# Kernel optimization log

Hardware: AMD Instinct MI355X
Metric: run time of the kernel (lower is better)

The kernel has to match this reference:

```python
import jax, jax.numpy as jnp
import numpy as np

B, S, D = 2, 2048, 2048
H, HKV = 16, 2
DH = D // H          # 128
G = H // HKV         # 8
SCALE = float(np.sqrt(DH))


def setup_inputs() -> dict:
    key = jax.random.key(0)
    ks = jax.random.split(key, 9)
    s = 0.02
    return {
        "x":  jax.random.normal(ks[0], (B, S, D), dtype=jnp.float32),
        "Wq": jax.random.normal(ks[1], (H * DH, D), dtype=jnp.float32) * s,
        "bq": jnp.zeros((H * DH,), dtype=jnp.float32),
        "Wk": jax.random.normal(ks[2], (HKV * DH, D), dtype=jnp.float32) * s,
        "bk": jnp.zeros((HKV * DH,), dtype=jnp.float32),
        "Wv": jax.random.normal(ks[3], (HKV * DH, D), dtype=jnp.float32) * s,
        "bv": jnp.zeros((HKV * DH,), dtype=jnp.float32),
        "Wo": jax.random.normal(ks[4], (D, D), dtype=jnp.float32) * s,
        "bo": jnp.zeros((D,), dtype=jnp.float32),
    }


def reference(x, Wq, bq, Wk, bk, Wv, bv, Wo, bo):
    # projections (torch Linear: y = x @ W.T + b)
    q = (x @ Wq.T + bq).reshape(B, S, HKV, G, DH)   # grouped query heads
    k = (x @ Wk.T + bk).reshape(B, S, HKV, DH)
    v = (x @ Wv.T + bv).reshape(B, S, HKV, DH)

    # scores: [B, HKV, G, S, S]; native grouping (no KV expand/copy)
    scores = jnp.einsum('bskgd,btkd->bkgst', q, k) / SCALE

    causal = jnp.triu(jnp.ones((S, S), dtype=bool), k=1)
    scores = jnp.where(causal, -jnp.inf, scores)
    attn = jax.nn.softmax(scores, axis=-1)          # dropout = identity (eval)

    out = jnp.einsum('bkgst,btkd->bskgd', attn, v).reshape(B, S, D)
    return out @ Wo.T + bo
```

## Files before the change

### kernel.cpp

```cpp
#include <hip/hip_runtime.h>
#include <hip/hip_bf16.h>
#include <cmath>
#include <stdint.h>

#define B_ 2
#define S_ 2048
#define D_ 2048
#define H_ 16
#define HKV_ 2
#define DH_ 128
#define G_ 8
#define DKV_ 256
#define NQKV_ 2560

typedef _Float16 f16;
typedef _Float16 f16x8 __attribute__((ext_vector_type(8)));
typedef _Float16 f16x4 __attribute__((ext_vector_type(4)));
typedef float f32x4 __attribute__((ext_vector_type(4)));

__device__ __forceinline__ void gload_lds16(const void* g, void* lds) {
  __builtin_amdgcn_global_load_lds((const __attribute__((address_space(1))) void*)g,
                                   (__attribute__((address_space(3))) void*)lds,
                                   16, 0, 0);
}

__device__ __forceinline__ float fexp2(float x) {
  float r;
  asm("v_exp_f32 %0, %1" : "=v"(r) : "v"(x));
  return r;
}

__global__ void prep_kernel(const float* __restrict__ x,  const float* __restrict__ Wq,
                            const float* __restrict__ Wk, const float* __restrict__ Wv,
                            const float* __restrict__ Wo, const float* __restrict__ bq,
                            const float* __restrict__ bk, const float* __restrict__ bv,
                            f16* __restrict__ xh, f16* __restrict__ wqkv,
                            f16* __restrict__ woh, float* __restrict__ bqkv) {
  constexpr int N0 = 2097152;
  constexpr int N1 = N0 + 1048576;
  constexpr int N2 = N1 + 131072;
  constexpr int N3 = N2 + 131072;
  constexpr int N4 = N3 + 1048576;
  constexpr int N5 = N4 + 512;
  constexpr int N6 = N5 + 64;
  constexpr int N7 = N6 + 64;
  int i = blockIdx.x * blockDim.x + threadIdx.x;
  const int stride = gridDim.x * blockDim.x;
  for (; i < N7; i += stride) {
    if (i < N4) {
      const float* s; f16x4* d; int j;
      if (i < N0)      { s = x;  d = (f16x4*)xh;             j = i; }
      else if (i < N1) { s = Wq; d = (f16x4*)wqkv;           j = i - N0; }
      else if (i < N2) { s = Wk; d = (f16x4*)wqkv + 1048576; j = i - N1; }
      else if (i < N3) { s = Wv; d = (f16x4*)wqkv + 1179648; j = i - N2; }
      else             { s = Wo; d = (f16x4*)woh;            j = i - N3; }
      float4 v = reinterpret_cast<const float4*>(s)[j];
      f16x4 o = { (f16)v.x, (f16)v.y, (f16)v.z, (f16)v.w };
      d[j] = o;
    } else {
      const float* s; int off, j;
      if (i < N5)      { s = bq; off = 0;   j = i - N4; }
      else if (i < N6) { s = bk; off = 512; j = i - N5; }
      else             { s = bv; off = 576; j = i - N6; }
      reinterpret_cast<float4*>(bqkv)[off + j] = reinterpret_cast<const float4*>(s)[j];
    }
  }
}

template<int EPI>
__global__ __launch_bounds__(256)
void gemm_core(const f16* __restrict__ A, const f16* __restrict__ Bm,
               const float* __restrict__ bias,
               f16* __restrict__ oQ, f16* __restrict__ oK, f16* __restrict__ oV,
               float* __restrict__ oF,
               int M, int N, int K, int nbx) {
  __shared__ __align__(16) f16 sA[128 * 64];
  __shared__ __align__(16) f16 sB[128 * 64];
  const int tid  = threadIdx.x;
  const int lane = tid & 63;
  const int w    = tid >> 6;
  const int wr   = w >> 1, wc = w & 1;
  const int r16  = lane & 15, grp = lane >> 4;
  const int nwg  = gridDim.x;
  const int cpx  = nwg >> 3;
  const int lg   = (blockIdx.x & 7) * cpx + (blockIdx.x >> 3);
  const int bm   = (lg / nbx) * 128;
  const int bn   = (lg % nbx) * 128;

  f32x4 acc[4][4] = {};

  auto stage = [&](int k0) {
#pragma unroll
    for (int j = 0; j < 4; ++j) {
      int seg = j * 4 + w;
      int rr  = seg * 8 + (lane >> 3);
      int cs  = lane & 7;
      int csr = (cs ^ (rr & 7)) * 8;
      gload_lds16(A  + (size_t)(bm + rr) * K + k0 + csr, &sA[seg * 512]);
      gload_lds16(Bm + (size_t)(bn + rr) * K + k0 + csr, &sB[seg * 512]);
    }
  };

  const int nk = K >> 6;
  for (int t = 0; t < nk; ++t) {
    stage(t << 6);
    asm volatile("s_waitcnt vmcnt(0)" ::: "memory");
    __builtin_amdgcn_s_barrier();

#pragma unroll
    for (int kk = 0; kk < 64; kk += 32) {
      f16x8 af[4], bf[4];
      const int cb = (kk >> 3) + grp;
      const int cx = (cb ^ (r16 & 7)) << 3;
#pragma unroll
      for (int m = 0; m < 4; ++m)
        af[m] = *reinterpret_cast<const f16x8*>(&sA[(wr * 64 + m * 16 + r16) * 64 + cx]);
#pragma unroll
      for (int n = 0; n < 4; ++n)
        bf[n] = *reinterpret_cast<const f16x8*>(&sB[(wc * 64 + n * 16 + r16) * 64 + cx]);
#pragma unroll
      for (int m = 0; m < 4; ++m)
#pragma unroll
        for (int n = 0; n < 4; ++n)
          acc[m][n] = __builtin_amdgcn_mfma_f32_16x16x32_f16(af[m], bf[n], acc[m][n], 0, 0, 0);
    }

    __builtin_amdgcn_s_barrier();
  }

#pragma unroll
  for (int n = 0; n < 4; ++n) {
    int col = bn + wc * 64 + n * 16 + r16;
    float bv = bias ? bias[col] : 0.f;
#pragma unroll
    for (int m = 0; m < 4; ++m) {
      int row0 = bm + wr * 64 + m * 16 + grp * 4;
      if constexpr (EPI == 0) {
#pragma unroll
        for (int j = 0; j < 4; ++j)
          oF[(size_t)(row0 + j) * N + col] = acc[m][n][j] + bv;
      } else {
        if (bn < 2048) {
#pragma unroll
          for (int j = 0; j < 4; ++j)
            oQ[(size_t)(row0 + j) * 2048 + col] = (f16)(acc[m][n][j] + bv);
        } else if (bn < 2304) {
#pragma unroll
          for (int j = 0; j < 4; ++j)
            oK[(size_t)(row0 + j) * 256 + (col - 2048)] = (f16)(acc[m][n][j] + bv);
        } else {
          f16x4 st;
#pragma unroll
          for (int j = 0; j < 4; ++j) st[j] = (f16)(acc[m][n][j] + bv);
          *reinterpret_cast<f16x4*>(&oV[(size_t)(row0 >> 2) * 1024 + (col - 2304) * 4]) = st;
        }
      }
    }
  }
}

__global__ __launch_bounds__(256)
void attn_kernel(const f16* __restrict__ Q, const f16* __restrict__ K,
                 const f16* __restrict__ V4, f16* __restrict__ O) {
  __shared__ __align__(16) f16 sK[2][8192];
  __shared__ __align__(16) f16 sV[2][8192];

  const int tid  = threadIdx.x;
  const int lane = tid & 63;
  const int w    = tid >> 6;
  const int qi   = lane & 15, grp = lane >> 4;
  const int bid  = blockIdx.x;
  const int hh   = bid & 1;
  const int kvh  = (bid >> 1) & 1;
  const int b    = (bid >> 2) & 1;
  const int j    = bid >> 3;
  const int hq   = kvh * 8 + hh * 4 + w;
  const f16 SCL2 = (f16)(0.08838834764831845f * 1.44269504088896f);

  const f16* Kb = K  + (size_t)b * S_ * DKV_ + kvh * DH_;
  const f16* Vb = V4 + (size_t)b * S_ * DKV_ + kvh * 512;

  auto stage = [&](int t64, int buf) {
#pragma unroll
    for (int p4 = 0; p4 < 4; ++p4) {
      int ci = p4 * 256 + tid;
      int r = ci >> 4, cs = ci & 15;
      gload_lds16(Kb + (size_t)(t64 * 64 + r) * DKV_ + ((cs ^ (r & 7)) * 8),
                  (char*)&sK[buf][0] + p4 * 4096 + w * 1024);
      int g = ci >> 6, cc = ci & 63;
      gload_lds16(Vb + (size_t)(t64 * 16 + g) * 1024 + ((cc ^ g) * 8),
                  (char*)&sV[buf][0] + p4 * 4096 + w * 1024);
    }
  };

  const int q2    = qi >> 1;
  const int voff0 = ((q2 ^ grp) << 3) + (qi & 1) * 4;
  const int voff1 = ((q2 ^ (grp + 4)) << 3) + (qi & 1) * 4;

  for (int task = 0; task < 2; ++task) {
    const int qt    = task ? j : (127 - j);
    const int nt    = (qt >> 2) + 1;
    const int q_pos = qt * 16 + qi;

    const size_t qbase = ((size_t)(b * S_ + qt * 16 + qi)) * D_ + hq * DH_;
    f16x8 qf[4];
#pragma unroll
    for (int kd = 0; kd < 4; ++kd) {
      qf[kd] = *reinterpret_cast<const f16x8*>(Q + qbase + kd * 32 + grp * 8);
#pragma unroll
      for (int e = 0; e < 8; ++e) qf[kd][e] *= SCL2;
    }

    float m = -INFINITY, lsum = 0.f;
    f32x4 accO[8] = {};

    auto tile_step = [&](const f16* sKb, const f16* sVb, int kv0, bool MASK) {
      f32x4 s0 = {}, s1 = {}, s2 = {}, s3 = {};
#pragma unroll
      for (int kd = 0; kd < 4; ++kd) {
        const int cx = ((kd * 4 + grp) ^ (qi & 7)) << 3;
        f16x8 k0 = *reinterpret_cast<const f16x8*>(sKb + qi * 128 + cx);
        f16x8 k1 = *reinterpret_cast<const f16x8*>(sKb + (16 + qi) * 128 + cx);
        f16x8 k2 = *reinterpret_cast<const f16x8*>(sKb + (32 + qi) * 128 + cx);
        f16x8 k3 = *reinterpret_cast<const f16x8*>(sKb + (48 + qi) * 128 + cx);
        s0 = __builtin_amdgcn_mfma_f32_16x16x32_f16(k0, qf[kd], s0, 0, 0, 0);
        s1 = __builtin_amdgcn_mfma_f32_16x16x32_f16(k1, qf[kd], s1, 0, 0, 0);
        s2 = __builtin_amdgcn_mfma_f32_16x16x32_f16(k2, qf[kd], s2, 0, 0, 0);
        s3 = __builtin_amdgcn_mfma_f32_16x16x32_f16(k3, qf[kd], s3, 0, 0, 0);
      }
      float p[16];
#pragma unroll
      for (int jj = 0; jj < 4; ++jj) {
        p[jj] = s0[jj]; p[4 + jj] = s1[jj]; p[8 + jj] = s2[jj]; p[12 + jj] = s3[jj];
      }
      if (MASK) {
#pragma unroll
        for (int qd = 0; qd < 4; ++qd)
#pragma unroll
          for (int jj = 0; jj < 4; ++jj) {
            int kvp = kv0 + qd * 16 + grp * 4 + jj;
            p[qd * 4 + jj] = (kvp > q_pos) ? -INFINITY : p[qd * 4 + jj];
          }
      }
      float a0 = fmaxf(p[0], p[8]),  a1 = fmaxf(p[1], p[9]);
      float a2 = fmaxf(p[2], p[10]), a3 = fmaxf(p[3], p[11]);
      float a4 = fmaxf(p[4], p[12]), a5 = fmaxf(p[5], p[13]);
      float a6 = fmaxf(p[6], p[14]), a7 = fmaxf(p[7], p[15]);
      a0 = fmaxf(a0, a4); a1 = fmaxf(a1, a5); a2 = fmaxf(a2, a6); a3 = fmaxf(a3, a7);
      a0 = fmaxf(a0, a2); a1 = fmaxf(a1, a3);
      float tm = fmaxf(a0, a1);
      if (!__all(tm <= m + 8.f)) {
        float r = tm;
        r = fmaxf(r, __shfl_xor(r, 16));
        r = fmaxf(r, __shfl_xor(r, 32));
        float mn = fmaxf(m, r);
        float sc = fexp2(m - mn);
        m = mn;
        lsum *= sc;
#pragma unroll
        for (int dt = 0; dt < 8; ++dt)
#pragma unroll
          for (int jj = 0; jj < 4; ++jj) accO[dt][jj] *= sc;
      }
      float ps = 0.f;
#pragma unroll
      for (int i = 0; i < 16; ++i) {
        p[i] = fexp2(p[i] - m);
        ps += p[i];
      }
      lsum += ps;

      f16x4 pf0 = { (f16)p[0],  (f16)p[1],  (f16)p[2],  (f16)p[3]  };
      f16x4 pf1 = { (f16)p[4],  (f16)p[5],  (f16)p[6],  (f16)p[7]  };
      f16x4 pf2 = { (f16)p[8],  (f16)p[9],  (f16)p[10], (f16)p[11] };
      f16x4 pf3 = { (f16)p[12], (f16)p[13], (f16)p[14], (f16)p[15] };
      const f16* vb0 = sVb + grp * 512 + voff0;
      const f16* vb1 = sVb + (grp + 4) * 512 + voff1;
      const f16* vb2 = sVb + (8 + grp) * 512 + voff0;
      const f16* vb3 = sVb + (12 + grp) * 512 + voff1;
#pragma unroll
      for (int dtp = 0; dtp < 8; ++dtp) {
        const int dt1 = dtp ^ 1;
        f16x4 v0 = *reinterpret_cast<const f16x4*>(vb0 + dtp * 64);
        f16x4 v1 = *reinterpret_cast<const f16x4*>(vb1 + dtp * 64);
        f16x4 v2 = *reinterpret_cast<const f16x4*>(vb2 + dtp * 64);
        f16x4 v3 = *reinterpret_cast<const f16x4*>(vb3 + dtp * 64);
        accO[dtp] = __builtin_amdgcn_mfma_f32_16x16x16f16(v0, pf0, accO[dtp], 0, 0, 0);
        accO[dtp] = __builtin_amdgcn_mfma_f32_16x16x16f16(v1, pf1, accO[dtp], 0, 0, 0);
        accO[dt1] = __builtin_amdgcn_mfma_f32_16x16x16f16(v2, pf2, accO[dt1], 0, 0, 0);
        accO[dt1] = __builtin_amdgcn_mfma_f32_16x16x16f16(v3, pf3, accO[dt1], 0, 0, 0);
      }
    };

    stage(0, 0);
    asm volatile("s_waitcnt vmcnt(0)" ::: "memory");
    __builtin_amdgcn_s_barrier();

    for (int t = 0; t < nt - 1; ++t) {
      const int buf = t & 1;
      stage(t + 1, buf ^ 1);
      tile_step(&sK[buf][0], &sV[buf][0], t * 64, false);
      asm volatile("s_waitcnt vmcnt(0)" ::: "memory");
      __builtin_amdgcn_s_barrier();
    }

    {
      const int t = nt - 1, buf = t & 1;
      tile_step(&sK[buf][0], &sV[buf][0], t * 64, true);
    }

    lsum += __shfl_xor(lsum, 16);
    lsum += __shfl_xor(lsum, 32);
    float inv_l = 1.f / lsum;
    const size_t obase = ((size_t)(b * S_ + qt * 16 + qi)) * D_ + hq * DH_;
#pragma unroll
    for (int dt = 0; dt < 8; ++dt) {
      f16x4 st;
#pragma unroll
      for (int jj = 0; jj < 4; ++jj) st[jj] = (f16)(accO[dt][jj] * inv_l);
      *reinterpret_cast<f16x4*>(&O[obase + dt * 16 + grp * 4]) = st;
    }
    __builtin_amdgcn_s_barrier();
  }
}

extern "C" void kernel_launch(void* const* d_in, const int* in_sizes, int n_in,
                              void* d_out, int out_size, void* d_ws, size_t ws_size,
                              hipStream_t stream) {
  const float* x  = (const float*)d_in[0];
  const float* Wq = (const float*)d_in[1];
  const float* bq = (const float*)d_in[2];
  const float* Wk = (const float*)d_in[3];
  const float* bk = (const float*)d_in[4];
  const float* Wv = (const float*)d_in[5];
  const float* bv = (const float*)d_in[6];
  const float* Wo = (const float*)d_in[7];
  const float* bo = (const float*)d_in[8];
  float* out = (float*)d_out;

  char* ws = (char*)d_ws;
  size_t off = 0;
  auto alloc = [&](size_t bytes) {
    char* p = ws + off;
    off += (bytes + 255) & ~(size_t)255;
    return p;
  };
  f16*   xh    = (f16*)alloc((size_t)B_ * S_ * D_ * 2);
  f16*   wqkv  = (f16*)alloc((size_t)NQKV_ * D_ * 2);
  f16*   woh   = (f16*)alloc((size_t)D_ * D_ * 2);
  f16*   qh    = (f16*)alloc((size_t)B_ * S_ * D_ * 2);
  f16*   kh    = (f16*)alloc((size_t)B_ * S_ * DKV_ * 2);
  f16*   v4h   = (f16*)alloc((size_t)B_ * S_ * DKV_ * 2);
  f16*   ah    = (f16*)alloc((size_t)B_ * S_ * D_ * 2);
  float* bqkv  = (float*)alloc((size_t)NQKV_ * 4);

  prep_kernel<<<dim3(2048), dim3(256), 0, stream>>>(
      x, Wq, Wk, Wv, Wo, bq, bk, bv, xh, wqkv, woh, bqkv);

  const int M = B_ * S_;
  gemm_core<1><<<dim3((M / 128) * (NQKV_ / 128)), 256, 0, stream>>>(
      xh, wqkv, bqkv, qh, kh, v4h, nullptr, M, NQKV_, D_, NQKV_ / 128);

  attn_kernel<<<dim3(512), 256, 0, stream>>>(qh, kh, v4h, ah);

  gemm_core<0><<<dim3((M / 128) * (D_ / 128)), 256, 0, stream>>>(
      ah, woh, bo, nullptr, nullptr, nullptr, out, M, D_, D_, D_ / 128);
}
```

Measured before the change: 184.5 us.

## Process two query heads per wave to reuse K/V tiles across heads

Each wave now handles two query heads of the same KV group. The K and V fragments read from shared memory feed both heads' MFMAs, so each block stages a KV tile once for all 8 grouped heads instead of twice. The per-block pair of complementary causal tasks is dropped. Instead the block index is remapped so one block handles one query tile, with long and short tiles interleaved across the grid. This halves LDS reads and global K/V traffic per head, at the cost of doubling accumulator registers (which may lower occupancy) and giving up the explicit per-block causal load balancing.

```diff
diff --git a/kernel.cpp b/kernel.cpp
--- a/kernel.cpp
+++ b/kernel.cpp
@@ -170,11 +170,12 @@
   const int w    = tid >> 6;
   const int qi   = lane & 15, grp = lane >> 4;
   const int bid  = blockIdx.x;
-  const int hh   = bid & 1;
-  const int kvh  = (bid >> 1) & 1;
-  const int b    = (bid >> 2) & 1;
-  const int j    = bid >> 3;
-  const int hq   = kvh * 8 + hh * 4 + w;
+  const int b    = (bid >> 1) & 1;
+  const int kvh  = (bid >> 2) & 1;
+  const int v_   = ((bid >> 3) & 31) * 2 + (bid & 1);
+  const int qt   = (bid & 256) ? (127 - v_) : v_;
+  const int hqA  = kvh * 8 + w;
+  const int hqB  = kvh * 8 + 4 + w;
   const f16 SCL2 = (f16)(0.08838834764831845f * 1.44269504088896f);
 
   const f16* Kb = K  + (size_t)b * S_ * DKV_ + kvh * DH_;
@@ -197,130 +198,157 @@
   const int voff0 = ((q2 ^ grp) << 3) + (qi & 1) * 4;
   const int voff1 = ((q2 ^ (grp + 4)) << 3) + (qi & 1) * 4;
 
-  for (int task = 0; task < 2; ++task) {
-    const int qt    = task ? j : (127 - j);
-    const int nt    = (qt >> 2) + 1;
-    const int q_pos = qt * 16 + qi;
-
-    const size_t qbase = ((size_t)(b * S_ + qt * 16 + qi)) * D_ + hq * DH_;
-    f16x8 qf[4];
+  const int nt    = (qt >> 2) + 1;
+  const int q_pos = qt * 16 + qi;
+
+  const size_t qrow = ((size_t)(b * S_ + qt * 16 + qi)) * D_;
+  f16x8 qfA[4], qfB[4];
+#pragma unroll
+  for (int kd = 0; kd < 4; ++kd) {
+    qfA[kd] = *reinterpret_cast<const f16x8*>(Q + qrow + hqA * DH_ + kd * 32 + grp * 8);
+    qfB[kd] = *reinterpret_cast<const f16x8*>(Q + qrow + hqB * DH_ + kd * 32 + grp * 8);
+#pragma unroll
+    for (int e = 0; e < 8; ++e) { qfA[kd][e] *= SCL2; qfB[kd][e] *= SCL2; }
+  }
+
+  float mA = -INFINITY, lsA = 0.f;
+  float mB = -INFINITY, lsB = 0.f;
+  f32x4 accA[8] = {}, accB[8] = {};
+
+  auto tile_step = [&](const f16* sKb, const f16* sVb, int kv0, bool MASK) {
+    f32x4 sA0 = {}, sA1 = {}, sA2 = {}, sA3 = {};
+    f32x4 sB0 = {}, sB1 = {}, sB2 = {}, sB3 = {};
 #pragma unroll
     for (int kd = 0; kd < 4; ++kd) {
-      qf[kd] = *reinterpret_cast<const f16x8*>(Q + qbase + kd * 32 + grp * 8);
-#pragma unroll
-      for (int e = 0; e < 8; ++e) qf[kd][e] *= SCL2;
-    }
-
-    float m = -INFINITY, lsum = 0.f;
-    f32x4 accO[8] = {};
-
-    auto tile_step = [&](const f16* sKb, const f16* sVb, int kv0, bool MASK) {
-      f32x4 s0 = {}, s1 = {}, s2 = {}, s3 = {};
-#pragma unroll
-      for (int kd = 0; kd < 4; ++kd) {
-        const int cx = ((kd * 4 + grp) ^ (qi & 7)) << 3;
-        f16x8 k0 = *reinterpret_cast<const f16x8*>(sKb + qi * 128 + cx);
-        f16x8 k1 = *reinterpret_cast<const f16x8*>(sKb + (16 + qi) * 128 + cx);
-        f16x8 k2 = *reinterpret_cast<const f16x8*>(sKb + (32 + qi) * 128 + cx);
-        f16x8 k3 = *reinterpret_cast<const f16x8*>(sKb + (48 + qi) * 128 + cx);
-        s0 = __builtin_amdgcn_mfma_f32_16x16x32_f16(k0, qf[kd], s0, 0, 0, 0);
-        s1 = __builtin_amdgcn_mfma_f32_16x16x32_f16(k1, qf[kd], s1, 0, 0, 0);
-        s2 = __builtin_amdgcn_mfma_f32_16x16x32_f16(k2, qf[kd], s2, 0, 0, 0);
-        s3 = __builtin_amdgcn_mfma_f32_16x16x32_f16(k3, qf[kd], s3, 0, 0, 0);
-      }
-      float p[16];
-#pragma unroll
-      for (int jj = 0; jj < 4; ++jj) {
-        p[jj] = s0[jj]; p[4 + jj] = s1[jj]; p[8 + jj] = s2[jj]; p[12 + jj] = s3[jj];
-      }
-      if (MASK) {
-#pragma unroll
-        for (int qd = 0; qd < 4; ++qd)
-#pragma unroll
-          for (int jj = 0; jj < 4; ++jj) {
-            int kvp = kv0 + qd * 16 + grp * 4 + jj;
-            p[qd * 4 + jj] = (kvp > q_pos) ? -INFINITY : p[qd * 4 + jj];
-          }
-      }
-      float a0 = fmaxf(p[0], p[8]),  a1 = fmaxf(p[1], p[9]);
-      float a2 = fmaxf(p[2], p[10]), a3 = fmaxf(p[3], p[11]);
-      float a4 = fmaxf(p[4], p[12]), a5 = fmaxf(p[5], p[13]);
-      float a6 = fmaxf(p[6], p[14]), a7 = fmaxf(p[7], p[15]);
+      const int cx = ((kd * 4 + grp) ^ (qi & 7)) << 3;
+      f16x8 k0 = *reinterpret_cast<const f16x8*>(sKb + qi * 128 + cx);
+      f16x8 k1 = *reinterpret_cast<const f16x8*>(sKb + (16 + qi) * 128 + cx);
+      f16x8 k2 = *reinterpret_cast<const f16x8*>(sKb + (32 + qi) * 128 + cx);
+      f16x8 k3 = *reinterpret_cast<const f16x8*>(sKb + (48 + qi) * 128 + cx);
+      sA0 = __builtin_amdgcn_mfma_f32_16x16x32_f16(k0, qfA[kd], sA0, 0, 0, 0);
+      sB0 = __builtin_amdgcn_mfma_f32_16x16x32_f16(k0, qfB[kd], sB0, 0, 0, 0);
+      sA1 = __builtin_amdgcn_mfma_f32_16x16x32_f16(k1, qfA[kd], sA1, 0, 0, 0);
+      sB1 = __builtin_amdgcn_mfma_f32_16x16x32_f16(k1, qfB[kd], sB1, 0, 0, 0);
+      sA2 = __builtin_amdgcn_mfma_f32_16x16x32_f16(k2, qfA[kd], sA2, 0, 0, 0);
+      sB2 = __builtin_amdgcn_mfma_f32_16x16x32_f16(k2, qfB[kd], sB2, 0, 0, 0);
+      sA3 = __builtin_amdgcn_mfma_f32_16x16x32_f16(k3, qfA[kd], sA3, 0, 0, 0);
+      sB3 = __builtin_amdgcn_mfma_f32_16x16x32_f16(k3, qfB[kd], sB3, 0, 0, 0);
+    }
+    float pA[16], pB[16];
+#pragma unroll
+    for (int jj = 0; jj < 4; ++jj) {
+      pA[jj] = sA0[jj]; pA[4 + jj] = sA1[jj]; pA[8 + jj] = sA2[jj]; pA[12 + jj] = sA3[jj];
+      pB[jj] = sB0[jj]; pB[4 + jj] = sB1[jj]; pB[8 + jj] = sB2[jj]; pB[12 + jj] = sB3[jj];
+    }
+    if (MASK) {
+#pragma unroll
+      for (int qd = 0; qd < 4; ++qd)
+#pragma unroll
+        for (int jj = 0; jj < 4; ++jj) {
+          int kvp = kv0 + qd * 16 + grp * 4 + jj;
+          bool msk = kvp > q_pos;
+          pA[qd * 4 + jj] = msk ? -INFINITY : pA[qd * 4 + jj];
+          pB[qd * 4 + jj] = msk ? -INFINITY : pB[qd * 4 + jj];
+        }
+    }
+    float tmA, tmB;
+    {
+      float a0 = fmaxf(pA[0], pA[8]),  a1 = fmaxf(pA[1], pA[9]);
+      float a2 = fmaxf(pA[2], pA[10]), a3 = fmaxf(pA[3], pA[11]);
+      float a4 = fmaxf(pA[4], pA[12]), a5 = fmaxf(pA[5], pA[13]);
+      float a6 = fmaxf(pA[6], pA[14]), a7 = fmaxf(pA[7], pA[15]);
       a0 = fmaxf(a0, a4); a1 = fmaxf(a1, a5); a2 = fmaxf(a2, a6); a3 = fmaxf(a3, a7);
-      a0 = fmaxf(a0, a2); a1 = fmaxf(a1, a3);
-      float tm = fmaxf(a0, a1);
-      if (!__all(tm <= m + 8.f)) {
-        float r = tm;
-        r = fmaxf(r, __shfl_xor(r, 16));
-        r = fmaxf(r, __shfl_xor(r, 32));
-        float mn = fmaxf(m, r);
-        float sc = fexp2(m - mn);
-        m = mn;
-        lsum *= sc;
-#pragma unroll
-        for (int dt = 0; dt < 8; ++dt)
-#pragma unroll
-          for (int jj = 0; jj < 4; ++jj) accO[dt][jj] *= sc;
-      }
-      float ps = 0.f;
-#pragma unroll
-      for (int i = 0; i < 16; ++i) {
-        p[i] = fexp2(p[i] - m);
-        ps += p[i];
-      }
-      lsum += ps;
-
-      f16x4 pf0 = { (f16)p[0],  (f16)p[1],  (f16)p[2],  (f16)p[3]  };
-      f16x4 pf1 = { (f16)p[4],  (f16)p[5],  (f16)p[6],  (f16)p[7]  };
-      f16x4 pf2 = { (f16)p[8],  (f16)p[9],  (f16)p[10], (f16)p[11] };
-      f16x4 pf3 = { (f16)p[12], (f16)p[13], (f16)p[14], (f16)p[15] };
-      const f16* vb0 = sVb + grp * 512 + voff0;
-      const f16* vb1 = sVb + (grp + 4) * 512 + voff1;
-      const f16* vb2 = sVb + (8 + grp) * 512 + voff0;
-      const f16* vb3 = sVb + (12 + grp) * 512 + voff1;
-#pragma unroll
-      for (int dtp = 0; dtp < 8; ++dtp) {
-        const int dt1 = dtp ^ 1;
-        f16x4 v0 = *reinterpret_cast<const f16x4*>(vb0 + dtp * 64);
-        f16x4 v1 = *reinterpret_cast<const f16x4*>(vb1 + dtp * 64);
-        f16x4 v2 = *reinterpret_cast<const f16x4*>(vb2 + dtp * 64);
-        f16x4 v3 = *reinterpret_cast<const f16x4*>(vb3 + dtp * 64);
-        accO[dtp] = __builtin_amdgcn_mfma_f32_16x16x16f16(v0, pf0, accO[dtp], 0, 0, 0);
-        accO[dtp] = __builtin_amdgcn_mfma_f32_16x16x16f16(v1, pf1, accO[dtp], 0, 0, 0);
-        accO[dt1] = __builtin_amdgcn_mfma_f32_16x16x16f16(v2, pf2, accO[dt1], 0, 0, 0);
-        accO[dt1] = __builtin_amdgcn_mfma_f32_16x16x16f16(v3, pf3, accO[dt1], 0, 0, 0);
-      }
-    };
-
-    stage(0, 0);
+      tmA = fmaxf(fmaxf(a0, a2), fmaxf(a1, a3));
+      float b0 = fmaxf(pB[0], pB[8]),  b1 = fmaxf(pB[1], pB[9]);
+      float b2 = fmaxf(pB[2], pB[10]), b3 = fmaxf(pB[3], pB[11]);
+      float b4 = fmaxf(pB[4], pB[12]), b5 = fmaxf(pB[5], pB[13]);
+      float b6 = fmaxf(pB[6], pB[14]), b7 = fmaxf(pB[7], pB[15]);
+      b0 = fmaxf(b0, b4); b1 = fmaxf(b1, b5); b2 = fmaxf(b2, b6); b3 = fmaxf(b3, b7);
+      tmB = fmaxf(fmaxf(b0, b2), fmaxf(b1, b3));
+    }
+    if (!__all((tmA <= mA + 8.f) && (tmB <= mB + 8.f))) {
+      float rA = tmA, rB = tmB;
+      rA = fmaxf(rA, __shfl_xor(rA, 16)); rA = fmaxf(rA, __shfl_xor(rA, 32));
+      rB = fmaxf(rB, __shfl_xor(rB, 16)); rB = fmaxf(rB, __shfl_xor(rB, 32));
+      float mnA = fmaxf(mA, rA), mnB = fmaxf(mB, rB);
+      float scA = fexp2(mA - mnA), scB = fexp2(mB - mnB);
+      mA = mnA; mB = mnB;
+      lsA *= scA; lsB *= scB;
+#pragma unroll
+      for (int dt = 0; dt < 8; ++dt)
+#pragma unroll
+        for (int jj = 0; jj < 4; ++jj) { accA[dt][jj] *= scA; accB[dt][jj] *= scB; }
+    }
+    float psA = 0.f, psB = 0.f;
+#pragma unroll
+    for (int i = 0; i < 16; ++i) {
+      pA[i] = fexp2(pA[i] - mA); psA += pA[i];
+      pB[i] = fexp2(pB[i] - mB); psB += pB[i];
+    }
+    lsA += psA; lsB += psB;
+
+    f16x4 pfA0 = { (f16)pA[0],  (f16)pA[1],  (f16)pA[2],  (f16)pA[3]  };
+    f16x4 pfA1 = { (f16)pA[4],  (f16)pA[5],  (f16)pA[6],  (f16)pA[7]  };
+    f16x4 pfA2 = { (f16)pA[8],  (f16)pA[9],  (f16)pA[10], (f16)pA[11] };
+    f16x4 pfA3 = { (f16)pA[12], (f16)pA[13], (f16)pA[14], (f16)pA[15] };
+    f16x4 pfB0 = { (f16)pB[0],  (f16)pB[1],  (f16)pB[2],  (f16)pB[3]  };
+    f16x4 pfB1 = { (f16)pB[4],  (f16)pB[5],  (f16)pB[6],  (f16)pB[7]  };
+    f16x4 pfB2 = { (f16)pB[8],  (f16)pB[9],  (f16)pB[10], (f16)pB[11] };
+    f16x4 pfB3 = { (f16)pB[12], (f16)pB[13], (f16)pB[14], (f16)pB[15] };
+    const f16* vb0 = sVb + grp * 512 + voff0;
+    const f16* vb1 = sVb + (grp + 4) * 512 + voff1;
+    const f16* vb2 = sVb + (8 + grp) * 512 + voff0;
+    const f16* vb3 = sVb + (12 + grp) * 512 + voff1;
+#pragma unroll
+    for (int dtp = 0; dtp < 8; ++dtp) {
+      const int dt1 = dtp ^ 1;
+      f16x4 v0 = *reinterpret_cast<const f16x4*>(vb0 + dtp * 64);
+      f16x4 v1 = *reinterpret_cast<const f16x4*>(vb1 + dtp * 64);
+      f16x4 v2 = *reinterpret_cast<const f16x4*>(vb2 + dtp * 64);
+      f16x4 v3 = *reinterpret_cast<const f16x4*>(vb3 + dtp * 64);
+      accA[dtp] = __builtin_amdgcn_mfma_f32_16x16x16f16(v0, pfA0, accA[dtp], 0, 0, 0);
+      accB[dtp] = __builtin_amdgcn_mfma_f32_16x16x16f16(v0, pfB0, accB[dtp], 0, 0, 0);
+      accA[dtp] = __builtin_amdgcn_mfma_f32_16x16x16f16(v1, pfA1, accA[dtp], 0, 0, 0);
+      accB[dtp] = __builtin_amdgcn_mfma_f32_16x16x16f16(v1, pfB1, accB[dtp], 0, 0, 0);
+      accA[dt1] = __builtin_amdgcn_mfma_f32_16x16x16f16(v2, pfA2, accA[dt1], 0, 0, 0);
+      accB[dt1] = __builtin_amdgcn_mfma_f32_16x16x16f16(v2, pfB2, accB[dt1], 0, 0, 0);
+      accA[dt1] = __builtin_amdgcn_mfma_f32_16x16x16f16(v3, pfA3, accA[dt1], 0, 0, 0);
+      accB[dt1] = __builtin_amdgcn_mfma_f32_16x16x16f16(v3, pfB3, accB[dt1], 0, 0, 0);
+    }
+  };
+
+  stage(0, 0);
+  asm volatile("s_waitcnt vmcnt(0)" ::: "memory");
+  __builtin_amdgcn_s_barrier();
+
+  for (int t = 0; t < nt - 1; ++t) {
+    const int buf = t & 1;
+    stage(t + 1, buf ^ 1);
+    tile_step(&sK[buf][0], &sV[buf][0], t * 64, false);
     asm volatile("s_waitcnt vmcnt(0)" ::: "memory");
     __builtin_amdgcn_s_barrier();
-
-    for (int t = 0; t < nt - 1; ++t) {
-      const int buf = t & 1;
-      stage(t + 1, buf ^ 1);
-      tile_step(&sK[buf][0], &sV[buf][0], t * 64, false);
-      asm volatile("s_waitcnt vmcnt(0)" ::: "memory");
-      __builtin_amdgcn_s_barrier();
-    }
-
-    {
-      const int t = nt - 1, buf = t & 1;
-      tile_step(&sK[buf][0], &sV[buf][0], t * 64, true);
-    }
-
-    lsum += __shfl_xor(lsum, 16);
-    lsum += __shfl_xor(lsum, 32);
-    float inv_l = 1.f / lsum;
-    const size_t obase = ((size_t)(b * S_ + qt * 16 + qi)) * D_ + hq * DH_;
-#pragma unroll
-    for (int dt = 0; dt < 8; ++dt) {
-      f16x4 st;
-#pragma unroll
-      for (int jj = 0; jj < 4; ++jj) st[jj] = (f16)(accO[dt][jj] * inv_l);
-      *reinterpret_cast<f16x4*>(&O[obase + dt * 16 + grp * 4]) = st;
-    }
-    __builtin_amdgcn_s_barrier();
+  }
+
+  {
+    const int t = nt - 1, buf = t & 1;
+    tile_step(&sK[buf][0], &sV[buf][0], t * 64, true);
+  }
+
+  lsA += __shfl_xor(lsA, 16); lsA += __shfl_xor(lsA, 32);
+  lsB += __shfl_xor(lsB, 16); lsB += __shfl_xor(lsB, 32);
+  float ilA = 1.f / lsA, ilB = 1.f / lsB;
+  const size_t obA = qrow + hqA * DH_;
+  const size_t obB = qrow + hqB * DH_;
+#pragma unroll
+  for (int dt = 0; dt < 8; ++dt) {
+    f16x4 stA, stB;
+#pragma unroll
+    for (int jj = 0; jj < 4; ++jj) {
+      stA[jj] = (f16)(accA[dt][jj] * ilA);
+      stB[jj] = (f16)(accB[dt][jj] * ilB);
+    }
+    *reinterpret_cast<f16x4*>(&O[obA + dt * 16 + grp * 4]) = stA;
+    *reinterpret_cast<f16x4*>(&O[obB + dt * 16 + grp * 4]) = stB;
   }
 }
 
```

Result: slower. 189.7 us (+2.8%).
